# Optimization experiments

Measured on AMD Instinct MI355X. Metric: run time of the kernel, lower is better.

The kernel has to match this reference:

```python
import jax, jax.numpy as jnp
import numpy as np
import math

H = 768
NH = 12
D = H // NH


def setup_inputs() -> dict:
    key = jax.random.key(0)
    ks = jax.random.split(key, 13)
    B, S = 1, 384
    s = 0.02
    inp = {
        "hidden_states": jax.random.normal(ks[0], (B, S, H), jnp.float32),
        "attention_mask": jnp.zeros((B, 1, 1, S), jnp.float32),
        "pos_emb": jax.random.normal(ks[1], (B, S, S, H), jnp.float32),
        "Wq": jax.random.normal(ks[2], (H, H), jnp.float32) * s,
        "bq": jnp.zeros((H,), jnp.float32),
        "Wk": jax.random.normal(ks[3], (H, H), jnp.float32) * s,
        "bk": jnp.zeros((H,), jnp.float32),
        "Wv": jax.random.normal(ks[4], (H, H), jnp.float32) * s,
        "bv": jnp.zeros((H,), jnp.float32),
        "Wpk": jax.random.normal(ks[5], (H, H), jnp.float32) * s,
        "bpk": jnp.zeros((H,), jnp.float32),
        "Wpq": jax.random.normal(ks[6], (H, H), jnp.float32) * s,
        "bpq": jnp.zeros((H,), jnp.float32),
    }
    return inp


def reference(hidden_states, attention_mask, pos_emb,
              Wq, bq, Wk, bk, Wv, bv, Wpk, bpk, Wpq, bpq):
    B, S, Hd = hidden_states.shape
    split = lambda x: x.reshape(B, S, NH, D).transpose(0, 2, 1, 3)  # -> (B, h, S, d)
    q = split(hidden_states @ Wq + bq)
    k = split(hidden_states @ Wk + bk)
    v = split(hidden_states @ Wv + bv)

    # content-to-content
    c2c = jnp.einsum('bhid,bhjd->bhij', q, k)

    # per-pair position projections: (B,S,S,H) -> (B,S,S,h,d)
    pos_key = (pos_emb @ Wpk + bpk).reshape(B, S, S, NH, D)
    pos_query = (pos_emb @ Wpq + bpq).reshape(B, S, S, NH, D)

    # content-to-position: q[b,h,i,:] . pos_key[b,i,j,h,:]
    c2p = jnp.einsum('bhid,bijhd->bhij', q, pos_key)
    # position-to-content: pos_query[b,j,i,h,:] . k[b,h,j,:]
    p2c = jnp.einsum('bjihd,bhjd->bhij', pos_query, k)

    scores = (c2c + c2p + p2c) / math.sqrt(D) + attention_mask
    probs = jax.nn.softmax(scores, axis=-1)  # dropout is identity (p=0 / eval)
    ctx = jnp.einsum('bhij,bhjd->bhid', probs, v)
    return ctx.transpose(0, 2, 1, 3).reshape(B, S, Hd)
```

## Files before the change

### kernel.cpp

```cpp
#include <hip/hip_runtime.h>
#include <math.h>

#define SEQ 384
#define HDIM 768
#define NHEAD 12
#define DHEAD 64

__global__ __launch_bounds__(256)
void qkv_gemm(const float* __restrict__ X,
              const float* __restrict__ Wq, const float* __restrict__ bq,
              const float* __restrict__ Wk, const float* __restrict__ bk,
              const float* __restrict__ Wv, const float* __restrict__ bv,
              float* __restrict__ q, float* __restrict__ k, float* __restrict__ v)
{
    __shared__ float Xs[128 * 68];
    const int z = blockIdx.z;
    const float* W    = (z == 0) ? Wq : (z == 1) ? Wk : Wv;
    const float* bias = (z == 0) ? bq : (z == 1) ? bk : bv;
    float* out        = (z == 0) ? q  : (z == 1) ? k  : v;

    const int m0 = blockIdx.x * 64;
    const int n0 = blockIdx.y * 64;
    const int tid = threadIdx.x;
    const int ty = tid / 16, tx = tid % 16;

    const int lm = tid >> 2;
    const int lc = (tid & 3) * 4;

    float acc[4][4] = {};

    for (int k0 = 0; k0 < HDIM; k0 += 128) {
        float4 xa[8];
        #pragma unroll
        for (int it = 0; it < 8; it++)
            xa[it] = *(const float4*)&X[(size_t)(m0 + lm) * HDIM + k0 + it * 16 + lc];
        __syncthreads();
        #pragma unroll
        for (int it = 0; it < 8; it++) {
            const int kk = it * 16 + lc;
            Xs[(kk + 0) * 68 + lm] = xa[it].x;
            Xs[(kk + 1) * 68 + lm] = xa[it].y;
            Xs[(kk + 2) * 68 + lm] = xa[it].z;
            Xs[(kk + 3) * 68 + lm] = xa[it].w;
        }
        __syncthreads();
        const float* Wp = &W[(size_t)k0 * HDIM + n0 + 4 * tx];
        #pragma unroll 8
        for (int kk = 0; kk < 128; kk++) {
            float4 b4 = *(const float4*)&Wp[(size_t)kk * HDIM];
            float4 a4 = *(const float4*)&Xs[kk * 68 + 4 * ty];
            float a[4] = {a4.x, a4.y, a4.z, a4.w};
            float b[4] = {b4.x, b4.y, b4.z, b4.w};
            #pragma unroll
            for (int ia = 0; ia < 4; ia++)
                #pragma unroll
                for (int ib = 0; ib < 4; ib++)
                    acc[ia][ib] = fmaf(a[ia], b[ib], acc[ia][ib]);
        }
    }
    float4 bv4 = *(const float4*)&bias[n0 + 4 * tx];
    #pragma unroll
    for (int ia = 0; ia < 4; ia++) {
        float4 o;
        o.x = acc[ia][0] + bv4.x; o.y = acc[ia][1] + bv4.y;
        o.z = acc[ia][2] + bv4.z; o.w = acc[ia][3] + bv4.w;
        *(float4*)&out[(size_t)(m0 + 4 * ty + ia) * HDIM + n0 + 4 * tx] = o;
    }
}

__global__ __launch_bounds__(256)
void pos_proj(const float* __restrict__ q, const float* __restrict__ k,
              const float* __restrict__ Wpk, const float* __restrict__ Wpq,
              float* __restrict__ qp, float* __restrict__ kp)
{
    __shared__ float As[64][68];
    __shared__ float Bs[64][68];
    const int h = blockIdx.z % NHEAD;
    const int s = blockIdx.z / NHEAD;
    const float* Asrc = s ? k   : q;
    const float* Wsrc = s ? Wpq : Wpk;
    float* out        = s ? kp  : qp;

    const int i0 = blockIdx.x * 64, e0 = blockIdx.y * 64;
    const int tid = threadIdx.x;
    const int dg = tid % 16, row = tid / 16;

    #pragma unroll
    for (int r = 0; r < 4; r++) {
        const int rr = r * 16 + row;
        float4 a4 = *(const float4*)&Asrc[(size_t)(i0 + rr) * HDIM + h * 64 + dg * 4];
        float4 b4 = *(const float4*)&Wsrc[(size_t)(e0 + rr) * HDIM + h * 64 + dg * 4];
        As[dg * 4 + 0][rr] = a4.x; As[dg * 4 + 1][rr] = a4.y;
        As[dg * 4 + 2][rr] = a4.z; As[dg * 4 + 3][rr] = a4.w;
        Bs[dg * 4 + 0][rr] = b4.x; Bs[dg * 4 + 1][rr] = b4.y;
        Bs[dg * 4 + 2][rr] = b4.z; Bs[dg * 4 + 3][rr] = b4.w;
    }
    __syncthreads();

    const int ty = tid / 16, tx = tid % 16;
    float acc[4][4] = {};
    #pragma unroll 4
    for (int d = 0; d < 64; d++) {
        float4 a4 = *(const float4*)&As[d][4 * ty];
        float4 b4 = *(const float4*)&Bs[d][4 * tx];
        float a[4] = {a4.x, a4.y, a4.z, a4.w};
        float b[4] = {b4.x, b4.y, b4.z, b4.w};
        #pragma unroll
        for (int ia = 0; ia < 4; ia++)
            #pragma unroll
            for (int ib = 0; ib < 4; ib++)
                acc[ia][ib] = fmaf(a[ia], b[ib], acc[ia][ib]);
    }
    #pragma unroll
    for (int ia = 0; ia < 4; ia++) {
        float4 o = make_float4(acc[ia][0], acc[ia][1], acc[ia][2], acc[ia][3]);
        *(float4*)&out[((size_t)(i0 + 4 * ty + ia) * NHEAD + h) * HDIM + e0 + 4 * tx] = o;
    }
}

__global__ __launch_bounds__(256)
void scores_pos(const float* __restrict__ pe, const float* __restrict__ qp,
                const float* __restrict__ kp,
                float* __restrict__ A1, float* __restrict__ P2T)
{
    __shared__ float lds[32 * 200];
    const int i    = blockIdx.x;
    const int jh   = blockIdx.y;
    const int tid  = threadIdx.x;
    const int lane = tid & 63;
    const int wave = tid >> 6;
    const int rgu = __builtin_amdgcn_readfirstlane(wave >> 1);
    const int esu = __builtin_amdgcn_readfirstlane(wave & 1);

    const float* pebase = pe + ((size_t)i * SEQ + jh * 192) * HDIM;
    const float* wb = (rgu ? kp : qp) + (size_t)i * NHEAD * HDIM;

    const int wr  = tid >> 3;
    const int wec = tid & 7;

    float acc[12][3] = {};

    for (int c = 0; c < 24; c++) {
        const int e0 = c * 32;
        float4 g[6];
        #pragma unroll
        for (int rnd = 0; rnd < 3; rnd++) {
            const int jb = rnd * 64 + wr * 2;
            g[2 * rnd + 0] = *(const float4*)&pebase[(size_t)jb * HDIM + e0 + wec * 4];
            g[2 * rnd + 1] = *(const float4*)&pebase[(size_t)(jb + 1) * HDIM + e0 + wec * 4];
        }
        __syncthreads();
        #pragma unroll
        for (int rnd = 0; rnd < 3; rnd++) {
            const int jb = rnd * 64 + wr * 2;
            const float4 g0 = g[2 * rnd], g1 = g[2 * rnd + 1];
            *(float2*)&lds[(wec * 4 + 0) * 200 + jb] = make_float2(g0.x, g1.x);
            *(float2*)&lds[(wec * 4 + 1) * 200 + jb] = make_float2(g0.y, g1.y);
            *(float2*)&lds[(wec * 4 + 2) * 200 + jb] = make_float2(g0.z, g1.z);
            *(float2*)&lds[(wec * 4 + 3) * 200 + jb] = make_float2(g0.w, g1.w);
        }
        __syncthreads();
        const float* wc = wb + e0 + esu * 16;
        #pragma unroll 4
        for (int ee = 0; ee < 16; ee++) {
            const int ei = esu * 16 + ee;
            float2 p2 = *(const float2*)&lds[ei * 200 + 2 * lane];
            float  p1 = lds[ei * 200 + 128 + lane];
            #pragma unroll
            for (int r = 0; r < 12; r++) {
                const float w = wc[r * HDIM + ee];
                acc[r][0] = fmaf(w, p2.x, acc[r][0]);
                acc[r][1] = fmaf(w, p2.y, acc[r][1]);
                acc[r][2] = fmaf(w, p1,   acc[r][2]);
            }
        }
    }

    __syncthreads();
    if (esu == 1) {
        #pragma unroll
        for (int r = 0; r < 12; r++) {
            const int row = rgu * 12 + r;
            *(float2*)&lds[row * 200 + 2 * lane] = make_float2(acc[r][0], acc[r][1]);
            lds[row * 200 + 128 + lane] = acc[r][2];
        }
    }
    __syncthreads();
    if (esu == 0) {
        #pragma unroll
        for (int r = 0; r < 12; r++) {
            const int row = rgu * 12 + r;
            float2 o2 = *(const float2*)&lds[row * 200 + 2 * lane];
            float  o1 = lds[row * 200 + 128 + lane];
            o2.x += acc[r][0]; o2.y += acc[r][1]; o1 += acc[r][2];
            *(float2*)&lds[row * 200 + 2 * lane] = o2;
            lds[row * 200 + 128 + lane] = o1;
        }
    }
    __syncthreads();

    for (int t = tid; t < 24 * 48; t += 256) {
        const int row = t / 48;
        const int c4  = (t % 48) * 4;
        float4 o = *(const float4*)&lds[row * 200 + c4];
        float* dst = (row < 12)
            ? &A1[((size_t)row * SEQ + i) * SEQ + jh * 192 + c4]
            : &P2T[((size_t)(row - 12) * SEQ + i) * SEQ + jh * 192 + c4];
        *(float4*)dst = o;
    }
}

__global__ __launch_bounds__(384)
void attn_out(const float* __restrict__ A1, const float* __restrict__ P2T,
              const float* __restrict__ q, const float* __restrict__ k,
              const float* __restrict__ v,
              const float* __restrict__ bpk, const float* __restrict__ bpq,
              const float* __restrict__ mask, float* __restrict__ out)
{
    const int i = blockIdx.x, h = blockIdx.y;
    const int tid = threadIdx.x;
    __shared__ float q_s[64], bk_s[64], bq_s[64];
    __shared__ float p_s[SEQ];
    __shared__ float redm[6], reds[6];
    __shared__ float redvf[24 * 64];

    if (tid < 64)       q_s[tid]        = q[(size_t)i * HDIM + h * 64 + tid];
    else if (tid < 128) bk_s[tid - 64]  = bpk[h * 64 + tid - 64];
    else if (tid < 192) bq_s[tid - 128] = bpq[h * 64 + tid - 128];
    __syncthreads();

    const float* kr = k + (size_t)tid * HDIM + h * 64;
    float c2c = 0.f, kb = 0.f;
    #pragma unroll
    for (int dd = 0; dd < 16; dd++) {
        float4 k4 = *(const float4*)(kr + 4 * dd);
        c2c = fmaf(q_s[4 * dd + 0], k4.x, c2c);
        c2c = fmaf(q_s[4 * dd + 1], k4.y, c2c);
        c2c = fmaf(q_s[4 * dd + 2], k4.z, c2c);
        c2c = fmaf(q_s[4 * dd + 3], k4.w, c2c);
        kb  = fmaf(bq_s[4 * dd + 0], k4.x, kb);
        kb  = fmaf(bq_s[4 * dd + 1], k4.y, kb);
        kb  = fmaf(bq_s[4 * dd + 2], k4.z, kb);
        kb  = fmaf(bq_s[4 * dd + 3], k4.w, kb);
    }
    float qb = 0.f;
    #pragma unroll 8
    for (int d = 0; d < 64; d++) qb = fmaf(q_s[d], bk_s[d], qb);

    float sc = (A1[((size_t)h * SEQ + i) * SEQ + tid] +
                P2T[((size_t)h * SEQ + tid) * SEQ + i] +
                c2c + kb + qb) * 0.125f + mask[tid];

    const int lane = tid & 63, w = tid >> 6;
    float m = sc;
    #pragma unroll
    for (int o = 32; o; o >>= 1) m = fmaxf(m, __shfl_xor(m, o));
    if (lane == 0) redm[w] = m;
    __syncthreads();
    m = redm[0];
    #pragma unroll
    for (int t = 1; t < 6; t++) m = fmaxf(m, redm[t]);

    float p = __expf(sc - m);
    float sum = p;
    #pragma unroll
    for (int o = 32; o; o >>= 1) sum += __shfl_xor(sum, o);
    if (lane == 0) reds[w] = sum;
    p_s[tid] = p;
    __syncthreads();
    const float SUM = reds[0] + reds[1] + reds[2] + reds[3] + reds[4] + reds[5];

    const int dq = lane & 15, jsub = lane >> 4;
    const int j0 = w * 64;
    float4 av = make_float4(0.f, 0.f, 0.f, 0.f);
    #pragma unroll 8
    for (int jj = 0; jj < 16; jj++) {
        const int j = j0 + jj * 4 + jsub;
        float4 v4 = *(const float4*)&v[(size_t)j * HDIM + h * 64 + dq * 4];
        const float pj = p_s[j];
        av.x = fmaf(pj, v4.x, av.x); av.y = fmaf(pj, v4.y, av.y);
        av.z = fmaf(pj, v4.z, av.z); av.w = fmaf(pj, v4.w, av.w);
    }
    *(float4*)&redvf[(w * 4 + jsub) * 64 + dq * 4] = av;
    __syncthreads();
    if (tid < 64) {
        float o = 0.f;
        #pragma unroll
        for (int r = 0; r < 24; r++) o += redvf[r * 64 + tid];
        out[(size_t)i * HDIM + h * 64 + tid] = o / SUM;
    }
}

extern "C" void kernel_launch(void* const* d_in, const int* in_sizes, int n_in,
                              void* d_out, int out_size, void* d_ws, size_t ws_size,
                              hipStream_t stream)
{
    const float* hs   = (const float*)d_in[0];
    const float* mask = (const float*)d_in[1];
    const float* pe   = (const float*)d_in[2];
    const float* Wq   = (const float*)d_in[3];
    const float* bq   = (const float*)d_in[4];
    const float* Wk   = (const float*)d_in[5];
    const float* bk   = (const float*)d_in[6];
    const float* Wv   = (const float*)d_in[7];
    const float* bv   = (const float*)d_in[8];
    const float* Wpk  = (const float*)d_in[9];
    const float* bpk  = (const float*)d_in[10];
    const float* Wpq  = (const float*)d_in[11];
    const float* bpq  = (const float*)d_in[12];

    float* ws = (float*)d_ws;
    const size_t SZ_QKV = (size_t)SEQ * HDIM;
    const size_t SZ_QP  = (size_t)SEQ * NHEAD * HDIM;
    const size_t SZ_SC  = (size_t)NHEAD * SEQ * SEQ;
    float* q   = ws;
    float* k   = q  + SZ_QKV;
    float* v   = k  + SZ_QKV;
    float* qp  = v  + SZ_QKV;
    float* kp  = qp + SZ_QP;
    float* A1  = kp + SZ_QP;
    float* P2T = A1 + SZ_SC;

    qkv_gemm<<<dim3(6, 12, 3), 256, 0, stream>>>(hs, Wq, bq, Wk, bk, Wv, bv, q, k, v);
    pos_proj<<<dim3(6, 12, 24), 256, 0, stream>>>(q, k, Wpk, Wpq, qp, kp);
    scores_pos<<<dim3(SEQ, 2), 256, 0, stream>>>(pe, qp, kp, A1, P2T);
    attn_out<<<dim3(SEQ, NHEAD), 384, 0, stream>>>(A1, P2T, q, k, v, bpk, bpq, mask,
                                                   (float*)d_out);
}
```

Measured before the change: 848.9 us.

## Precompute content scores in tiled GEMM and double-buffer pos_emb loads

Adds a tiled cc_gemm kernel that computes (q+bpq)·(k+bpk) minus the bias product, then applies scale and mask. This replaces the per-row dot products that attn_out recomputed for every (i,h) block, and scores_pos now accumulates its c2p result into that buffer. The scores_pos main loop is restructured to double-buffer pos_emb chunks in registers, so global loads overlap with the FMA work, and the kernel gets an occupancy hint of 3 blocks. This costs extra register pressure, an additional kernel launch, and a read-modify-write of the CC buffer.

Result: faster. 791.1 us (-6.8%).

```diff
diff --git a/kernel.cpp b/kernel.cpp
--- a/kernel.cpp
+++ b/kernel.cpp
@@ -119,9 +119,69 @@
 }
 
 __global__ __launch_bounds__(256)
+void cc_gemm(const float* __restrict__ q, const float* __restrict__ k,
+             const float* __restrict__ bpq, const float* __restrict__ bpk,
+             const float* __restrict__ mask, float* __restrict__ CC)
+{
+    __shared__ float Qs[64][68];
+    __shared__ float Ks[64][68];
+    __shared__ float cterm_s;
+    const int h  = blockIdx.z;
+    const int i0 = blockIdx.x * 64, j0 = blockIdx.y * 64;
+    const int tid = threadIdx.x;
+    const int dg = tid % 16, row = tid / 16;
+
+    const float4 bq4 = *(const float4*)&bpq[h * 64 + dg * 4];
+    const float4 bk4 = *(const float4*)&bpk[h * 64 + dg * 4];
+    #pragma unroll
+    for (int r = 0; r < 4; r++) {
+        const int rr = r * 16 + row;
+        float4 q4 = *(const float4*)&q[(size_t)(i0 + rr) * HDIM + h * 64 + dg * 4];
+        float4 k4 = *(const float4*)&k[(size_t)(j0 + rr) * HDIM + h * 64 + dg * 4];
+        Qs[dg * 4 + 0][rr] = q4.x + bq4.x; Qs[dg * 4 + 1][rr] = q4.y + bq4.y;
+        Qs[dg * 4 + 2][rr] = q4.z + bq4.z; Qs[dg * 4 + 3][rr] = q4.w + bq4.w;
+        Ks[dg * 4 + 0][rr] = k4.x + bk4.x; Ks[dg * 4 + 1][rr] = k4.y + bk4.y;
+        Ks[dg * 4 + 2][rr] = k4.z + bk4.z; Ks[dg * 4 + 3][rr] = k4.w + bk4.w;
+    }
+    if (tid < 64) {
+        float pc = bpq[h * 64 + tid] * bpk[h * 64 + tid];
+        #pragma unroll
+        for (int o = 32; o; o >>= 1) pc += __shfl_xor(pc, o);
+        if (tid == 0) cterm_s = pc;
+    }
+    __syncthreads();
+
+    const int ty = tid / 16, tx = tid % 16;
+    float acc[4][4] = {};
+    #pragma unroll 4
+    for (int d = 0; d < 64; d++) {
+        float4 a4 = *(const float4*)&Qs[d][4 * ty];
+        float4 b4 = *(const float4*)&Ks[d][4 * tx];
+        float a[4] = {a4.x, a4.y, a4.z, a4.w};
+        float b[4] = {b4.x, b4.y, b4.z, b4.w};
+        #pragma unroll
+        for (int ia = 0; ia < 4; ia++)
+            #pragma unroll
+            for (int ib = 0; ib < 4; ib++)
+                acc[ia][ib] = fmaf(a[ia], b[ib], acc[ia][ib]);
+    }
+    const float cterm = cterm_s;
+    const float4 m4 = *(const float4*)&mask[j0 + 4 * tx];
+    #pragma unroll
+    for (int ia = 0; ia < 4; ia++) {
+        float4 o;
+        o.x = (acc[ia][0] - cterm) * 0.125f + m4.x;
+        o.y = (acc[ia][1] - cterm) * 0.125f + m4.y;
+        o.z = (acc[ia][2] - cterm) * 0.125f + m4.z;
+        o.w = (acc[ia][3] - cterm) * 0.125f + m4.w;
+        *(float4*)&CC[((size_t)h * SEQ + i0 + 4 * ty + ia) * SEQ + j0 + 4 * tx] = o;
+    }
+}
+
+__global__ __launch_bounds__(256, 3)
 void scores_pos(const float* __restrict__ pe, const float* __restrict__ qp,
                 const float* __restrict__ kp,
-                float* __restrict__ A1, float* __restrict__ P2T)
+                float* __restrict__ CC, float* __restrict__ P2T)
 {
     __shared__ float lds[32 * 200];
     const int i    = blockIdx.x;
@@ -139,17 +199,18 @@
     const int wec = tid & 7;
 
     float acc[12][3] = {};
-
-    for (int c = 0; c < 24; c++) {
+    float4 ga[6], gb[6];
+
+    auto loadc = [&](float4* g, int c) {
         const int e0 = c * 32;
-        float4 g[6];
         #pragma unroll
         for (int rnd = 0; rnd < 3; rnd++) {
             const int jb = rnd * 64 + wr * 2;
             g[2 * rnd + 0] = *(const float4*)&pebase[(size_t)jb * HDIM + e0 + wec * 4];
             g[2 * rnd + 1] = *(const float4*)&pebase[(size_t)(jb + 1) * HDIM + e0 + wec * 4];
         }
-        __syncthreads();
+    };
+    auto writec = [&](const float4* g) {
         #pragma unroll
         for (int rnd = 0; rnd < 3; rnd++) {
             const int jb = rnd * 64 + wr * 2;
@@ -159,8 +220,9 @@
             *(float2*)&lds[(wec * 4 + 2) * 200 + jb] = make_float2(g0.z, g1.z);
             *(float2*)&lds[(wec * 4 + 3) * 200 + jb] = make_float2(g0.w, g1.w);
         }
-        __syncthreads();
-        const float* wc = wb + e0 + esu * 16;
+    };
+    auto compute = [&](int c) {
+        const float* wc = wb + c * 32 + esu * 16;
         #pragma unroll 4
         for (int ee = 0; ee < 16; ee++) {
             const int ei = esu * 16 + ee;
@@ -174,6 +236,21 @@
                 acc[r][2] = fmaf(w, p1,   acc[r][2]);
             }
         }
+    };
+
+    loadc(ga, 0);
+    #pragma unroll 1
+    for (int cc = 0; cc < 12; cc++) {
+        loadc(gb, 2 * cc + 1);
+        __syncthreads();
+        writec(ga);
+        __syncthreads();
+        if (cc < 11) loadc(ga, 2 * cc + 2);
+        compute(2 * cc);
+        __syncthreads();
+        writec(gb);
+        __syncthreads();
+        compute(2 * cc + 1);
     }
 
     __syncthreads();
@@ -203,53 +280,30 @@
         const int row = t / 48;
         const int c4  = (t % 48) * 4;
         float4 o = *(const float4*)&lds[row * 200 + c4];
-        float* dst = (row < 12)
-            ? &A1[((size_t)row * SEQ + i) * SEQ + jh * 192 + c4]
-            : &P2T[((size_t)(row - 12) * SEQ + i) * SEQ + jh * 192 + c4];
-        *(float4*)dst = o;
+        o.x *= 0.125f; o.y *= 0.125f; o.z *= 0.125f; o.w *= 0.125f;
+        if (row < 12) {
+            float* dst = &CC[((size_t)row * SEQ + i) * SEQ + jh * 192 + c4];
+            float4 c = *(const float4*)dst;
+            c.x += o.x; c.y += o.y; c.z += o.z; c.w += o.w;
+            *(float4*)dst = c;
+        } else {
+            *(float4*)&P2T[((size_t)(row - 12) * SEQ + i) * SEQ + jh * 192 + c4] = o;
+        }
     }
 }
 
 __global__ __launch_bounds__(384)
-void attn_out(const float* __restrict__ A1, const float* __restrict__ P2T,
-              const float* __restrict__ q, const float* __restrict__ k,
-              const float* __restrict__ v,
-              const float* __restrict__ bpk, const float* __restrict__ bpq,
-              const float* __restrict__ mask, float* __restrict__ out)
+void attn_out(const float* __restrict__ CC, const float* __restrict__ P2T,
+              const float* __restrict__ v, float* __restrict__ out)
 {
     const int i = blockIdx.x, h = blockIdx.y;
     const int tid = threadIdx.x;
-    __shared__ float q_s[64], bk_s[64], bq_s[64];
     __shared__ float p_s[SEQ];
     __shared__ float redm[6], reds[6];
     __shared__ float redvf[24 * 64];
 
-    if (tid < 64)       q_s[tid]        = q[(size_t)i * HDIM + h * 64 + tid];
-    else if (tid < 128) bk_s[tid - 64]  = bpk[h * 64 + tid - 64];
-    else if (tid < 192) bq_s[tid - 128] = bpq[h * 64 + tid - 128];
-    __syncthreads();
-
-    const float* kr = k + (size_t)tid * HDIM + h * 64;
-    float c2c = 0.f, kb = 0.f;
-    #pragma unroll
-    for (int dd = 0; dd < 16; dd++) {
-        float4 k4 = *(const float4*)(kr + 4 * dd);
-        c2c = fmaf(q_s[4 * dd + 0], k4.x, c2c);
-        c2c = fmaf(q_s[4 * dd + 1], k4.y, c2c);
-        c2c = fmaf(q_s[4 * dd + 2], k4.z, c2c);
-        c2c = fmaf(q_s[4 * dd + 3], k4.w, c2c);
-        kb  = fmaf(bq_s[4 * dd + 0], k4.x, kb);
-        kb  = fmaf(bq_s[4 * dd + 1], k4.y, kb);
-        kb  = fmaf(bq_s[4 * dd + 2], k4.z, kb);
-        kb  = fmaf(bq_s[4 * dd + 3], k4.w, kb);
-    }
-    float qb = 0.f;
-    #pragma unroll 8
-    for (int d = 0; d < 64; d++) qb = fmaf(q_s[d], bk_s[d], qb);
-
-    float sc = (A1[((size_t)h * SEQ + i) * SEQ + tid] +
-                P2T[((size_t)h * SEQ + tid) * SEQ + i] +
-                c2c + kb + qb) * 0.125f + mask[tid];
+    float sc = CC[((size_t)h * SEQ + i) * SEQ + tid]
+             + P2T[((size_t)h * SEQ + tid) * SEQ + i];
 
     const int lane = tid & 63, w = tid >> 6;
     float m = sc;
@@ -318,12 +372,12 @@
     float* v   = k  + SZ_QKV;
     float* qp  = v  + SZ_QKV;
     float* kp  = qp + SZ_QP;
-    float* A1  = kp + SZ_QP;
-    float* P2T = A1 + SZ_SC;
+    float* P2T = kp + SZ_QP;
+    float* CC  = P2T + SZ_SC;
 
     qkv_gemm<<<dim3(6, 12, 3), 256, 0, stream>>>(hs, Wq, bq, Wk, bk, Wv, bv, q, k, v);
+    cc_gemm<<<dim3(6, 6, 12), 256, 0, stream>>>(q, k, bpq, bpk, mask, CC);
     pos_proj<<<dim3(6, 12, 24), 256, 0, stream>>>(q, k, Wpk, Wpq, qp, kp);
-    scores_pos<<<dim3(SEQ, 2), 256, 0, stream>>>(pe, qp, kp, A1, P2T);
-    attn_out<<<dim3(SEQ, NHEAD), 384, 0, stream>>>(A1, P2T, q, k, v, bpk, bpq, mask,
-                                                   (float*)d_out);
-}
+    scores_pos<<<dim3(SEQ, 2), 256, 0, stream>>>(pe, qp, kp, CC, P2T);
+    attn_out<<<dim3(SEQ, NHEAD), 384, 0, stream>>>(CC, P2T, v, (float*)d_out);
+}
```
